# Performance work log

Hardware: AMD Instinct MI355X
Metric: run time of the kernel (lower is better)

The kernel has to match this reference:

```python
import jax, jax.numpy as jnp
import numpy as np

B, C, H, W = 64, 64, 64, 64
KD = 64  # kernel_dim == res == dim (required by the torch reshapes)


def _ln(t, g, b, eps=1e-5):
    mu = jnp.mean(t, axis=-1, keepdims=True)
    var = jnp.var(t, axis=-1, keepdims=True)
    return (t - mu) * jax.lax.rsqrt(var + eps) * g + b


def _cos_map(n, kd):
    i = jnp.arange(n, dtype=jnp.float32)[:, None]
    j = jnp.arange(kd, dtype=jnp.float32)[None, :]
    return jnp.cos(i * j * jnp.pi / n) / kd


def setup_inputs() -> dict:
    key = jax.random.key(0)
    ks = jax.random.split(key, 6)
    s = 0.02
    return {
        "x": jax.random.normal(ks[0], (B, C, H, W), jnp.float32),
        "freq_embed": jax.random.normal(ks[1], (H, W, C), jnp.float32),
        "g_k": jnp.ones((C,), jnp.float32), "b_k": jnp.zeros((C,), jnp.float32),
        "Wk": jax.random.normal(ks[2], (C, KD), jnp.float32) * s, "bk": jnp.zeros((KD,), jnp.float32),
        "g_z": jnp.ones((C,), jnp.float32), "b_z": jnp.zeros((C,), jnp.float32),
        "Wz": jax.random.normal(ks[3], (C, C), jnp.float32) * s, "bz": jnp.zeros((C,), jnp.float32),
        "g_o": jnp.ones((KD,), jnp.float32), "b_o": jnp.zeros((KD,), jnp.float32),
        "Wo": jax.random.normal(ks[4], (KD, C), jnp.float32) * s, "bo": jnp.zeros((C,), jnp.float32),
    }


def reference(x, freq_embed, g_k, b_k, Wk, bk, g_z, b_z, Wz, bz, g_o, b_o, Wo, bo):
    # x: (B,C,H,W) -> (B,H,W,C), matching the torch permute branch
    x = jnp.transpose(x, (0, 2, 3, 1))
    Bc, Hc, Wc, Cc = x.shape
    kd = Wk.shape[1]
    xin = x + freq_embed[None]                    # freq_embed broadcast over batch
    k = _ln(xin, g_k, b_k) @ Wk + bk              # (B,H,W,kd)
    z = _ln(freq_embed, g_z, b_z) @ Wz + bz       # to_k(freq_embed): (H,W,C)
    cosn = _cos_map(Hc, kd)                       # (H,kd)
    cosm = _cos_map(Wc, kd)                       # (W,kd)
    i = jnp.arange(Hc, dtype=jnp.float32)[:, None]
    j = jnp.arange(Wc, dtype=jnp.float32)[None, :]
    decay = (jnp.exp(-(i + j) / max(Hc, Wc)) / kd).astype(x.dtype)  # (H,W)
    wexp = decay[:, :, None] ** z                 # (H,W,C), decay > 0
    # separable forward DCT (two kernel-1 conv1d == two contractions)
    t = jnp.einsum('nh,bhwc->bnwc', cosn, k)
    t = jnp.einsum('mw,bnwc->bnmc', cosm, t)
    t = t * wexp[None]                            # exponential-decay spectral gate
    # separable inverse DCT
    t = jnp.einsum('nh,bnmc->bhmc', cosn, t)
    t = jnp.einsum('mw,bhmc->bhwc', cosm, t)
    out = _ln(t, g_o, b_o) * jax.nn.silu(z)[None]
    out = out @ Wo + bo
    return jnp.transpose(out, (0, 3, 1, 2))       # back to BCHW
```

## Files before the change

### kernel.cpp

```cpp
#include <hip/hip_runtime.h>


typedef __attribute__((ext_vector_type(8))) short short8;
typedef __attribute__((ext_vector_type(4))) float f32x4;
typedef __attribute__((ext_vector_type(4))) unsigned short us4;

__device__ __forceinline__ unsigned short bfhi(float f) {
    return (unsigned short)(__builtin_bit_cast(unsigned int, f) >> 16);
}
__device__ __forceinline__ float hif(float f) {
    return __builtin_bit_cast(float, __builtin_bit_cast(unsigned int, f) & 0xFFFF0000u);
}
__device__ __forceinline__ int swa(int row, int col) {
    return (row << 7) + (((col >> 3) ^ (row & 7)) << 4) + ((col & 7) << 1);
}
__device__ __forceinline__ short8 fragrd(const short* buf, int row, int kc) {
    int a = (row << 7) + ((kc ^ (row & 7)) << 4);
    return *(const short8*)((const char*)buf + a);
}

__device__ __forceinline__ void mm_block(const short* Ah, const short* Al,
                                         const short* Bh, const short* Bl,
                                         int m0, int n0, int l15, int q,
                                         f32x4 (&acc)[2][2]) {
    const f32x4 zero = {0.f, 0.f, 0.f, 0.f};
    acc[0][0] = zero; acc[0][1] = zero; acc[1][0] = zero; acc[1][1] = zero;
    #pragma unroll
    for (int kb = 0; kb < 2; ++kb) {
        int kc = (kb << 2) + q;
        short8 a0h = fragrd(Ah, m0 + l15, kc);
        short8 a0l = fragrd(Al, m0 + l15, kc);
        short8 a1h = fragrd(Ah, m0 + 16 + l15, kc);
        short8 a1l = fragrd(Al, m0 + 16 + l15, kc);
        short8 b0h = fragrd(Bh, n0 + l15, kc);
        short8 b0l = fragrd(Bl, n0 + l15, kc);
        short8 b1h = fragrd(Bh, n0 + 16 + l15, kc);
        short8 b1l = fragrd(Bl, n0 + 16 + l15, kc);
        acc[0][0] = __builtin_amdgcn_mfma_f32_16x16x32_bf16(a0h, b0h, acc[0][0], 0, 0, 0);
        acc[0][0] = __builtin_amdgcn_mfma_f32_16x16x32_bf16(a0h, b0l, acc[0][0], 0, 0, 0);
        acc[0][0] = __builtin_amdgcn_mfma_f32_16x16x32_bf16(a0l, b0h, acc[0][0], 0, 0, 0);
        acc[0][1] = __builtin_amdgcn_mfma_f32_16x16x32_bf16(a0h, b1h, acc[0][1], 0, 0, 0);
        acc[0][1] = __builtin_amdgcn_mfma_f32_16x16x32_bf16(a0h, b1l, acc[0][1], 0, 0, 0);
        acc[0][1] = __builtin_amdgcn_mfma_f32_16x16x32_bf16(a0l, b1h, acc[0][1], 0, 0, 0);
        acc[1][0] = __builtin_amdgcn_mfma_f32_16x16x32_bf16(a1h, b0h, acc[1][0], 0, 0, 0);
        acc[1][0] = __builtin_amdgcn_mfma_f32_16x16x32_bf16(a1h, b0l, acc[1][0], 0, 0, 0);
        acc[1][0] = __builtin_amdgcn_mfma_f32_16x16x32_bf16(a1l, b0h, acc[1][0], 0, 0, 0);
        acc[1][1] = __builtin_amdgcn_mfma_f32_16x16x32_bf16(a1h, b1h, acc[1][1], 0, 0, 0);
        acc[1][1] = __builtin_amdgcn_mfma_f32_16x16x32_bf16(a1h, b1l, acc[1][1], 0, 0, 0);
        acc[1][1] = __builtin_amdgcn_mfma_f32_16x16x32_bf16(a1l, b1h, acc[1][1], 0, 0, 0);
    }
}

__global__ __launch_bounds__(256) void k_pre1(
    const float* __restrict__ g_k, const float* __restrict__ b_k,
    const float* __restrict__ Wk, const float* __restrict__ bk,
    const float* __restrict__ g_z, const float* __restrict__ b_z,
    const float* __restrict__ Wz, const float* __restrict__ bz,
    const float* __restrict__ Wo,
    unsigned short* __restrict__ WkTh, unsigned short* __restrict__ WkTl,
    float* __restrict__ su_k, float* __restrict__ v_k,
    unsigned short* __restrict__ WzTh, unsigned short* __restrict__ WzTl,
    float* __restrict__ su_z, float* __restrict__ v_z,
    unsigned short* __restrict__ WoTh, unsigned short* __restrict__ WoTl,
    unsigned short* __restrict__ cos_hi, unsigned short* __restrict__ cos_lo) {
    int t = threadIdx.x;
    if (blockIdx.x < 16) {
        int n = blockIdx.x * 4 + (t >> 6);
        int c = t & 63;
        float wk = Wk[c * 64 + n];
        float a = g_k[c] * wk;
        WkTh[n * 64 + c] = bfhi(a);
        WkTl[n * 64 + c] = bfhi(a - hif(a));
        float sa = a, sv = b_k[c] * wk;
        #pragma unroll
        for (int off = 32; off > 0; off >>= 1) {
            sa += __shfl_xor(sa, off, 64);
            sv += __shfl_xor(sv, off, 64);
        }
        if (c == 0) { su_k[n] = sa; v_k[n] = sv + bk[n]; }
        float wz = Wz[c * 64 + n];
        float az = g_z[c] * wz;
        WzTh[n * 64 + c] = bfhi(az);
        WzTl[n * 64 + c] = bfhi(az - hif(az));
        float saz = az, svz = b_z[c] * wz;
        #pragma unroll
        for (int off = 32; off > 0; off >>= 1) {
            saz += __shfl_xor(saz, off, 64);
            svz += __shfl_xor(svz, off, 64);
        }
        if (c == 0) { su_z[n] = saz; v_z[n] = svz + bz[n]; }
        float wo = Wo[c * 64 + n];
        WoTh[n * 64 + c] = bfhi(wo);
        WoTl[n * 64 + c] = bfhi(wo - hif(wo));
    } else {
        int idx = (blockIdx.x - 16) * 256 + t;
        int i = idx >> 6, j = idx & 63;
        float ang = (float)(i * j) * 3.14159265358979323846f * (1.0f / 64.0f);
        float v = cosf(ang) * (1.0f / 64.0f);
        cos_hi[idx] = bfhi(v);
        cos_lo[idx] = bfhi(v - hif(v));
    }
}

__global__ __launch_bounds__(256) void k_pre2(
    const float* __restrict__ freq,
    const unsigned short* __restrict__ WzTh_g, const unsigned short* __restrict__ WzTl_g,
    const float* __restrict__ su_z, const float* __restrict__ v_z,
    float* __restrict__ siluzT, float* __restrict__ wexpT,
    float* __restrict__ freqT) {
    __shared__ short Ah[4096], Al[4096], Bh[4096], Bl[4096];
    __shared__ float muS[64], rsS[64];
    __shared__ float tile[64][65];
    int t = threadIdx.x;
    if (blockIdx.x < 64) {
        int h = blockIdx.x;
        #pragma unroll
        for (int p = 0; p < 2; ++p) {
            int e = t + p * 256;
            int row = e >> 3, ch = e & 7;
            int a = (row << 7) + (((ch ^ (row & 7)) << 4));
            *(uint4*)((char*)Bh + a) = *(const uint4*)&WzTh_g[row * 64 + ch * 8];
            *(uint4*)((char*)Bl + a) = *(const uint4*)&WzTl_g[row * 64 + ch * 8];
        }
        int w = t >> 2, c0 = (t & 3) << 4;
        float4 fr[4];
        float s1 = 0.f, s2 = 0.f;
        #pragma unroll
        for (int i = 0; i < 4; ++i) {
            fr[i] = *(const float4*)&freq[(h * 64 + w) * 64 + c0 + 4 * i];
            s1 += fr[i].x + fr[i].y + fr[i].z + fr[i].w;
            s2 += fr[i].x * fr[i].x + fr[i].y * fr[i].y + fr[i].z * fr[i].z + fr[i].w * fr[i].w;
        }
        s1 += __shfl_xor(s1, 1, 64); s1 += __shfl_xor(s1, 2, 64);
        s2 += __shfl_xor(s2, 1, 64); s2 += __shfl_xor(s2, 2, 64);
        float mu = s1 * (1.0f / 64.0f);
        float var = s2 * (1.0f / 64.0f) - mu * mu;
        float rs = rsqrtf(var + 1e-5f);
        if ((t & 3) == 0) { muS[w] = mu; rsS[w] = rs; }
        const float* fp = (const float*)fr;
        #pragma unroll
        for (int i = 0; i < 4; ++i) {
            us4 hv, lv;
            #pragma unroll
            for (int r = 0; r < 4; ++r) {
                float f = fp[i * 4 + r];
                hv[r] = bfhi(f);
                lv[r] = bfhi(f - hif(f));
            }
            int a = swa(w, c0 + 4 * i);
            *(us4*)((char*)Ah + a) = hv;
            *(us4*)((char*)Al + a) = lv;
        }
        __syncthreads();
        int lane = t & 63, wv = t >> 6;
        int q = lane >> 4, l15 = lane & 15;
        int m0 = (wv & 1) << 5, n0 = (wv >> 1) << 5;
        f32x4 acc[2][2];
        mm_block(Ah, Al, Bh, Bl, m0, n0, l15, q, acc);
        #pragma unroll
        for (int u = 0; u < 2; ++u) {
            int c = n0 + (u << 4) + l15;
            float suc = su_z[c], vc = v_z[c];
            #pragma unroll
            for (int ti = 0; ti < 2; ++ti) {
                int wb = m0 + (ti << 4) + (q << 2);
                float4 mu4 = *(const float4*)&muS[wb];
                float4 rs4 = *(const float4*)&rsS[wb];
                float4 sil, wx;
                #pragma unroll
                for (int r = 0; r < 4; ++r) {
                    float z = ((const float*)&rs4)[r] * (acc[ti][u][r] - ((const float*)&mu4)[r] * suc) + vc;
                    float lnd = -(float)(h + wb + r) * 0.015625f - 4.1588830833596718565f;
                    ((float*)&sil)[r] = z / (1.0f + expf(-z));
                    ((float*)&wx)[r] = expf(z * lnd);
                }
                int base = (c * 64 + h) * 64 + wb;
                *(float4*)&siluzT[base] = sil;
                *(float4*)&wexpT[base] = wx;
            }
        }
    } else {
        int h = blockIdx.x - 64;
        int w = t >> 2, c0 = (t & 3) << 4;
        #pragma unroll
        for (int i = 0; i < 4; ++i)
            *(float4*)&tile[w][c0 + 4 * i] = *(const float4*)&freq[(h * 64 + w) * 64 + c0 + 4 * i];
        __syncthreads();
        int w0 = (t & 15) << 2;
        #pragma unroll
        for (int p = 0; p < 4; ++p) {
            int c = (t >> 4) + 16 * p;
            float4 fv = make_float4(tile[w0][c], tile[w0 + 1][c], tile[w0 + 2][c], tile[w0 + 3][c]);
            *(float4*)&freqT[(c * 64 + h) * 64 + w0] = fv;
        }
    }
}

__global__ __launch_bounds__(256, 3) void k_k(
    const float* __restrict__ x, const float* __restrict__ freqT,
    const unsigned short* __restrict__ WkTh_g, const unsigned short* __restrict__ WkTl_g,
    const float* __restrict__ su_k, const float* __restrict__ v_k,
    float* __restrict__ planes) {
    __shared__ short Ah[4096], Al[4096], Bh[4096], Bl[4096];
    __shared__ __align__(16) float red1[16][68], red2[16][68];
    __shared__ float muS[64], rsS[64];
    int b = blockIdx.x >> 6, h = blockIdx.x & 63;
    int t = threadIdx.x;
    #pragma unroll
    for (int p = 0; p < 2; ++p) {
        int e = t + p * 256;
        int row = e >> 3, ch = e & 7;
        int a = (row << 7) + (((ch ^ (row & 7)) << 4));
        *(uint4*)((char*)Bh + a) = *(const uint4*)&WkTh_g[row * 64 + ch * 8];
        *(uint4*)((char*)Bl + a) = *(const uint4*)&WkTl_g[row * 64 + ch * 8];
    }
    int g = t >> 4, w0 = (t & 15) << 2, c0 = g << 2;
    const float* xb = x + (size_t)b * 262144 + h * 64;
    float4 vr[4];
    float4 s1 = {0,0,0,0}, s2 = {0,0,0,0};
    #pragma unroll
    for (int i = 0; i < 4; ++i) {
        int c = c0 + i;
        float4 xv = *(const float4*)&xb[c * 4096 + w0];
        float4 fv = *(const float4*)&freqT[c * 4096 + h * 64 + w0];
        xv.x += fv.x; xv.y += fv.y; xv.z += fv.z; xv.w += fv.w;
        vr[i] = xv;
        s1.x += xv.x; s1.y += xv.y; s1.z += xv.z; s1.w += xv.w;
        s2.x += xv.x * xv.x; s2.y += xv.y * xv.y; s2.z += xv.z * xv.z; s2.w += xv.w * xv.w;
    }
    const float* vp = (const float*)vr;
    #pragma unroll
    for (int j = 0; j < 4; ++j) {
        us4 hv, lv;
        #pragma unroll
        for (int r = 0; r < 4; ++r) {
            float f = vp[r * 4 + j];
            hv[r] = bfhi(f);
            lv[r] = bfhi(f - hif(f));
        }
        int a = swa(w0 + j, c0);
        *(us4*)((char*)Ah + a) = hv;
        *(us4*)((char*)Al + a) = lv;
    }
    *(float4*)&red1[g][w0] = s1;
    *(float4*)&red2[g][w0] = s2;
    __syncthreads();
    if (t < 64) {
        float a1 = 0.f, a2 = 0.f;
        #pragma unroll
        for (int j = 0; j < 16; ++j) { a1 += red1[j][t]; a2 += red2[j][t]; }
        float mu = a1 * (1.0f / 64.0f);
        float var = a2 * (1.0f / 64.0f) - mu * mu;
        muS[t] = mu; rsS[t] = rsqrtf(var + 1e-5f);
    }
    __syncthreads();
    int lane = t & 63, wv = t >> 6;
    int q = lane >> 4, l15 = lane & 15;
    int m0 = (wv & 1) << 5, n0 = (wv >> 1) << 5;
    f32x4 acc[2][2];
    mm_block(Ah, Al, Bh, Bl, m0, n0, l15, q, acc);
    #pragma unroll
    for (int u = 0; u < 2; ++u) {
        int n = n0 + (u << 4) + l15;
        float sun = su_k[n], vn = v_k[n];
        #pragma unroll
        for (int ti = 0; ti < 2; ++ti) {
            int wb = m0 + (ti << 4) + (q << 2);
            float4 mu4 = *(const float4*)&muS[wb];
            float4 rs4 = *(const float4*)&rsS[wb];
            float4 o;
            o.x = rs4.x * (acc[ti][u][0] - mu4.x * sun) + vn;
            o.y = rs4.y * (acc[ti][u][1] - mu4.y * sun) + vn;
            o.z = rs4.z * (acc[ti][u][2] - mu4.z * sun) + vn;
            o.w = rs4.w * (acc[ti][u][3] - mu4.w * sun) + vn;
            *(float4*)&planes[((size_t)(b * 64 + n) * 64 + h) * 64 + wb] = o;
        }
    }
}

__global__ __launch_bounds__(256, 3) void k_spec(
    float* __restrict__ planes,
    const unsigned short* __restrict__ cos_hi, const unsigned short* __restrict__ cos_lo,
    const float* __restrict__ wexpT) {
    __shared__ short Ch[4096], Cl[4096];
    __shared__ short D0h[4096], D0l[4096];
    __shared__ short D1h[4096], D1l[4096];
    int b = blockIdx.x >> 6, c = blockIdx.x & 63;
    float* po = planes + (size_t)(b * 64 + c) * 4096;
    int t = threadIdx.x;
    int lane = t & 63, wv = t >> 6;
    int q = lane >> 4, l15 = lane & 15;
    int m0 = (wv & 1) << 5, n0 = (wv >> 1) << 5;

    {
        int r = t >> 2, cb = (t & 3) << 4;
        #pragma unroll
        for (int p = 0; p < 2; ++p) {
            int chunk = (cb >> 3) + p;
            int a = (r << 7) + (((chunk ^ (r & 7)) << 4));
            *(uint4*)((char*)Ch + a) = *(const uint4*)&cos_hi[r * 64 + cb + p * 8];
            *(uint4*)((char*)Cl + a) = *(const uint4*)&cos_lo[r * 64 + cb + p * 8];
        }
    }
    {
        int w = t & 63, h0 = (t >> 6) << 4;
        float v[16];
        #pragma unroll
        for (int j = 0; j < 16; ++j) v[j] = po[(h0 + j) * 64 + w];
        #pragma unroll
        for (int g = 0; g < 4; ++g) {
            int col = h0 + (g << 2);
            int a = swa(w, col);
            us4 hv, lv;
            #pragma unroll
            for (int r = 0; r < 4; ++r) {
                float f = v[(g << 2) + r];
                hv[r] = bfhi(f);
                lv[r] = bfhi(f - hif(f));
            }
            *(us4*)((char*)D0h + a) = hv;
            *(us4*)((char*)D0l + a) = lv;
        }
    }
    __syncthreads();

    f32x4 acc[2][2];

#define WB_T(Dh, Dl)                                                                \
    {                                                                               \
        _Pragma("unroll")                                                           \
        for (int ti = 0; ti < 2; ++ti)                                              \
            _Pragma("unroll")                                                       \
            for (int u = 0; u < 2; ++u) {                                           \
                int row = n0 + (u << 4) + l15;                                      \
                int col = m0 + (ti << 4) + (q << 2);                                \
                int a = swa(row, col);                                              \
                us4 hv, lv;                                                         \
                _Pragma("unroll")                                                   \
                for (int r = 0; r < 4; ++r) {                                       \
                    float f = acc[ti][u][r];                                        \
                    hv[r] = bfhi(f);                                                \
                    lv[r] = bfhi(f - hif(f));                                       \
                }                                                                   \
                *(us4*)((char*)Dh + a) = hv;                                        \
                *(us4*)((char*)Dl + a) = lv;                                        \
            }                                                                       \
    }

    mm_block(D0h, D0l, Ch, Cl, m0, n0, l15, q, acc);
    WB_T(D1h, D1l)
    __syncthreads();
    mm_block(D1h, D1l, Ch, Cl, m0, n0, l15, q, acc);
    {
        const float* wx = wexpT + (size_t)c * 4096;
        #pragma unroll
        for (int ti = 0; ti < 2; ++ti)
            #pragma unroll
            for (int u = 0; u < 2; ++u)
                #pragma unroll
                for (int r = 0; r < 4; ++r) {
                    int n = m0 + (ti << 4) + (q << 2) + r;
                    int m = n0 + (u << 4) + l15;
                    acc[ti][u][r] *= wx[n * 64 + m];
                }
    }
    WB_T(D0h, D0l)
    __syncthreads();
    mm_block(Ch, Cl, D0h, D0l, m0, n0, l15, q, acc);
    {
        #pragma unroll
        for (int ti = 0; ti < 2; ++ti)
            #pragma unroll
            for (int u = 0; u < 2; ++u)
                #pragma unroll
                for (int r = 0; r < 4; ++r) {
                    int row = m0 + (ti << 4) + (q << 2) + r;
                    int col = n0 + (u << 4) + l15;
                    int a = swa(row, col);
                    float f = acc[ti][u][r];
                    *(unsigned short*)((char*)D1h + a) = bfhi(f);
                    *(unsigned short*)((char*)D1l + a) = bfhi(f - hif(f));
                }
    }
    __syncthreads();
    mm_block(D1h, D1l, Ch, Cl, m0, n0, l15, q, acc);
    {
        #pragma unroll
        for (int ti = 0; ti < 2; ++ti)
            #pragma unroll
            for (int u = 0; u < 2; ++u)
                #pragma unroll
                for (int r = 0; r < 4; ++r) {
                    int h = m0 + (ti << 4) + (q << 2) + r;
                    int w = n0 + (u << 4) + l15;
                    po[h * 64 + w] = acc[ti][u][r];
                }
    }
#undef WB_T
}

__global__ __launch_bounds__(256, 3) void k_out(
    const float* __restrict__ planes, const float* __restrict__ siluzT,
    const float* __restrict__ g_o, const float* __restrict__ b_o,
    const unsigned short* __restrict__ WoTh_g, const unsigned short* __restrict__ WoTl_g,
    const float* __restrict__ bo, float* __restrict__ out) {
    __shared__ short Ah[4096], Al[4096], Bh[4096], Bl[4096];
    __shared__ __align__(16) float red1[16][68], red2[16][68];
    __shared__ float muS[64], rsS[64];
    int b = blockIdx.x >> 6, h = blockIdx.x & 63;
    int t = threadIdx.x;
    #pragma unroll
    for (int p = 0; p < 2; ++p) {
        int e = t + p * 256;
        int row = e >> 3, ch = e & 7;
        int a = (row << 7) + (((ch ^ (row & 7)) << 4));
        *(uint4*)((char*)Bh + a) = *(const uint4*)&WoTh_g[row * 64 + ch * 8];
        *(uint4*)((char*)Bl + a) = *(const uint4*)&WoTl_g[row * 64 + ch * 8];
    }
    int g = t >> 4, w0 = (t & 15) << 2, c0 = g << 2;
    const float* pb = planes + (size_t)b * 262144 + h * 64;
    float4 vr[4], szr[4];
    float4 s1 = {0,0,0,0}, s2 = {0,0,0,0};
    #pragma unroll
    for (int i = 0; i < 4; ++i) {
        int c = c0 + i;
        float4 tv = *(const float4*)&pb[c * 4096 + w0];
        szr[i] = *(const float4*)&siluzT[c * 4096 + h * 64 + w0];
        vr[i] = tv;
        s1.x += tv.x; s1.y += tv.y; s1.z += tv.z; s1.w += tv.w;
        s2.x += tv.x * tv.x; s2.y += tv.y * tv.y; s2.z += tv.z * tv.z; s2.w += tv.w * tv.w;
    }
    *(float4*)&red1[g][w0] = s1;
    *(float4*)&red2[g][w0] = s2;
    __syncthreads();
    if (t < 64) {
        float a1 = 0.f, a2 = 0.f;
        #pragma unroll
        for (int j = 0; j < 16; ++j) { a1 += red1[j][t]; a2 += red2[j][t]; }
        float mu = a1 * (1.0f / 64.0f);
        float var = a2 * (1.0f / 64.0f) - mu * mu;
        muS[t] = mu; rsS[t] = rsqrtf(var + 1e-5f);
    }
    __syncthreads();
    {
        float4 mu4 = *(const float4*)&muS[w0];
        float4 rs4 = *(const float4*)&rsS[w0];
        #pragma unroll
        for (int i = 0; i < 4; ++i) {
            int c = c0 + i;
            float go = g_o[c], boc = b_o[c];
            vr[i].x = ((vr[i].x - mu4.x) * rs4.x * go + boc) * szr[i].x;
            vr[i].y = ((vr[i].y - mu4.y) * rs4.y * go + boc) * szr[i].y;
            vr[i].z = ((vr[i].z - mu4.z) * rs4.z * go + boc) * szr[i].z;
            vr[i].w = ((vr[i].w - mu4.w) * rs4.w * go + boc) * szr[i].w;
        }
        const float* vp = (const float*)vr;
        #pragma unroll
        for (int j = 0; j < 4; ++j) {
            us4 hv, lv;
            #pragma unroll
            for (int r = 0; r < 4; ++r) {
                float f = vp[r * 4 + j];
                hv[r] = bfhi(f);
                lv[r] = bfhi(f - hif(f));
            }
            int a = swa(w0 + j, c0);
            *(us4*)((char*)Ah + a) = hv;
            *(us4*)((char*)Al + a) = lv;
        }
    }
    __syncthreads();
    int lane = t & 63, wv = t >> 6;
    int q = lane >> 4, l15 = lane & 15;
    int m0 = (wv & 1) << 5, n0 = (wv >> 1) << 5;
    f32x4 acc[2][2];
    mm_block(Ah, Al, Bh, Bl, m0, n0, l15, q, acc);
    #pragma unroll
    for (int u = 0; u < 2; ++u) {
        int o_ = n0 + (u << 4) + l15;
        float bov = bo[o_];
        #pragma unroll
        for (int ti = 0; ti < 2; ++ti) {
            int wb = m0 + (ti << 4) + (q << 2);
            float4 o;
            o.x = acc[ti][u][0] + bov;
            o.y = acc[ti][u][1] + bov;
            o.z = acc[ti][u][2] + bov;
            o.w = acc[ti][u][3] + bov;
            *(float4*)&out[((size_t)(b * 64 + o_) * 64 + h) * 64 + wb] = o;
        }
    }
}

extern "C" void kernel_launch(void* const* d_in, const int* in_sizes, int n_in,
                              void* d_out, int out_size, void* d_ws, size_t ws_size,
                              hipStream_t stream) {
    const float* x    = (const float*)d_in[0];
    const float* freq = (const float*)d_in[1];
    const float* g_k  = (const float*)d_in[2];
    const float* b_k  = (const float*)d_in[3];
    const float* Wk   = (const float*)d_in[4];
    const float* bk   = (const float*)d_in[5];
    const float* g_z  = (const float*)d_in[6];
    const float* b_z  = (const float*)d_in[7];
    const float* Wz   = (const float*)d_in[8];
    const float* bz   = (const float*)d_in[9];
    const float* g_o  = (const float*)d_in[10];
    const float* b_o  = (const float*)d_in[11];
    const float* Wo   = (const float*)d_in[12];
    const float* bo   = (const float*)d_in[13];
    float* out = (float*)d_out;

    float* ws = (float*)d_ws;
    float* planes = ws;
    float* siluzT = planes + 16777216;
    float* wexpT  = siluzT + 262144;
    float* freqT  = wexpT + 262144;
    float* su_k   = freqT + 262144;
    float* v_k    = su_k + 64;
    float* su_z   = v_k + 64;
    float* v_z    = su_z + 64;
    unsigned short* cos_hi = (unsigned short*)(v_z + 64);
    unsigned short* cos_lo = cos_hi + 4096;
    unsigned short* WkTh = cos_lo + 4096;
    unsigned short* WkTl = WkTh + 4096;
    unsigned short* WzTh = WkTl + 4096;
    unsigned short* WzTl = WzTh + 4096;
    unsigned short* WoTh = WzTl + 4096;
    unsigned short* WoTl = WoTh + 4096;

    k_pre1<<<32, 256, 0, stream>>>(g_k, b_k, Wk, bk, g_z, b_z, Wz, bz, Wo,
                                   WkTh, WkTl, su_k, v_k, WzTh, WzTl, su_z, v_z,
                                   WoTh, WoTl, cos_hi, cos_lo);
    k_pre2<<<128, 256, 0, stream>>>(freq, WzTh, WzTl, su_z, v_z, siluzT, wexpT, freqT);
    k_k<<<4096, 256, 0, stream>>>(x, freqT, WkTh, WkTl, su_k, v_k, planes);
    k_spec<<<4096, 256, 0, stream>>>(planes, cos_hi, cos_lo, wexpT);
    k_out<<<4096, 256, 0, stream>>>(planes, siluzT, g_o, b_o, WoTh, WoTl, bo, out);
}
```

Before: 210.7 us.

## Move bf16 hi/lo split into k_k epilogue and shuffle-reduce LN stats in double

k_k now stores the k planes as packed bf16 hi/lo pairs, so k_spec only unpacks bits when loading instead of recomputing the split. The LayerNorm statistics in k_pre2, k_k and k_out are accumulated in double. In k_k and k_out a wavefront shuffle reduction feeds a small shared array, which removes one __syncthreads and the serial 64-thread reduction step. Occupancy hints for k_k and k_out are raised from 3 to 4. Double-precision arithmetic and shuffles add FP64 ALU cost, and the packed planes hold only the bf16 hi+lo precision.

```diff
diff --git a/kernel.cpp b/kernel.cpp
--- a/kernel.cpp
+++ b/kernel.cpp
@@ -10,6 +10,11 @@
 }
 __device__ __forceinline__ float hif(float f) {
     return __builtin_bit_cast(float, __builtin_bit_cast(unsigned int, f) & 0xFFFF0000u);
+}
+__device__ __forceinline__ unsigned int packsplit(float f) {
+    unsigned int h = (unsigned int)bfhi(f);
+    unsigned int l = (unsigned int)bfhi(f - hif(f));
+    return (h << 16) | l;
 }
 __device__ __forceinline__ int swa(int row, int col) {
     return (row << 7) + (((col >> 3) ^ (row & 7)) << 4) + ((col & 7) << 1);
@@ -124,19 +129,23 @@
         }
         int w = t >> 2, c0 = (t & 3) << 4;
         float4 fr[4];
-        float s1 = 0.f, s2 = 0.f;
+        double s1 = 0.0, s2 = 0.0;
         #pragma unroll
         for (int i = 0; i < 4; ++i) {
             fr[i] = *(const float4*)&freq[(h * 64 + w) * 64 + c0 + 4 * i];
-            s1 += fr[i].x + fr[i].y + fr[i].z + fr[i].w;
-            s2 += fr[i].x * fr[i].x + fr[i].y * fr[i].y + fr[i].z * fr[i].z + fr[i].w * fr[i].w;
+            const float* fp = (const float*)&fr[i];
+            #pragma unroll
+            for (int r = 0; r < 4; ++r) {
+                double d = (double)fp[r];
+                s1 += d; s2 += d * d;
+            }
         }
         s1 += __shfl_xor(s1, 1, 64); s1 += __shfl_xor(s1, 2, 64);
         s2 += __shfl_xor(s2, 1, 64); s2 += __shfl_xor(s2, 2, 64);
-        float mu = s1 * (1.0f / 64.0f);
-        float var = s2 * (1.0f / 64.0f) - mu * mu;
-        float rs = rsqrtf(var + 1e-5f);
-        if ((t & 3) == 0) { muS[w] = mu; rsS[w] = rs; }
+        double mu = s1 * (1.0 / 64.0);
+        double var = s2 * (1.0 / 64.0) - mu * mu;
+        float rs = rsqrtf((float)(var + 1e-5));
+        if ((t & 3) == 0) { muS[w] = (float)mu; rsS[w] = rs; }
         const float* fp = (const float*)fr;
         #pragma unroll
         for (int i = 0; i < 4; ++i) {
@@ -196,16 +205,17 @@
     }
 }
 
-__global__ __launch_bounds__(256, 3) void k_k(
+__global__ __launch_bounds__(256, 4) void k_k(
     const float* __restrict__ x, const float* __restrict__ freqT,
     const unsigned short* __restrict__ WkTh_g, const unsigned short* __restrict__ WkTl_g,
     const float* __restrict__ su_k, const float* __restrict__ v_k,
-    float* __restrict__ planes) {
+    unsigned int* __restrict__ planes) {
     __shared__ short Ah[4096], Al[4096], Bh[4096], Bl[4096];
-    __shared__ __align__(16) float red1[16][68], red2[16][68];
-    __shared__ float muS[64], rsS[64];
+    __shared__ double red1[4][64], red2[4][64];
     int b = blockIdx.x >> 6, h = blockIdx.x & 63;
     int t = threadIdx.x;
+    int lane = t & 63, wv = t >> 6;
+    int q = lane >> 4, l15 = lane & 15;
     #pragma unroll
     for (int p = 0; p < 2; ++p) {
         int e = t + p * 256;
@@ -217,7 +227,7 @@
     int g = t >> 4, w0 = (t & 15) << 2, c0 = g << 2;
     const float* xb = x + (size_t)b * 262144 + h * 64;
     float4 vr[4];
-    float4 s1 = {0,0,0,0}, s2 = {0,0,0,0};
+    double s1[4] = {0,0,0,0}, s2[4] = {0,0,0,0};
     #pragma unroll
     for (int i = 0; i < 4; ++i) {
         int c = c0 + i;
@@ -225,8 +235,27 @@
         float4 fv = *(const float4*)&freqT[c * 4096 + h * 64 + w0];
         xv.x += fv.x; xv.y += fv.y; xv.z += fv.z; xv.w += fv.w;
         vr[i] = xv;
-        s1.x += xv.x; s1.y += xv.y; s1.z += xv.z; s1.w += xv.w;
-        s2.x += xv.x * xv.x; s2.y += xv.y * xv.y; s2.z += xv.z * xv.z; s2.w += xv.w * xv.w;
+        const float* xp = (const float*)&xv;
+        #pragma unroll
+        for (int r = 0; r < 4; ++r) {
+            double d = (double)xp[r];
+            s1[r] += d; s2[r] += d * d;
+        }
+    }
+    #pragma unroll
+    for (int off = 16; off <= 32; off <<= 1) {
+        #pragma unroll
+        for (int r = 0; r < 4; ++r) {
+            s1[r] += __shfl_xor(s1[r], off, 64);
+            s2[r] += __shfl_xor(s2[r], off, 64);
+        }
+    }
+    if (q == 0) {
+        #pragma unroll
+        for (int r = 0; r < 4; ++r) {
+            red1[wv][(l15 << 2) + r] = s1[r];
+            red2[wv][(l15 << 2) + r] = s2[r];
+        }
     }
     const float* vp = (const float*)vr;
     #pragma unroll
@@ -242,51 +271,47 @@
         *(us4*)((char*)Ah + a) = hv;
         *(us4*)((char*)Al + a) = lv;
     }
-    *(float4*)&red1[g][w0] = s1;
-    *(float4*)&red2[g][w0] = s2;
-    __syncthreads();
-    if (t < 64) {
-        float a1 = 0.f, a2 = 0.f;
-        #pragma unroll
-        for (int j = 0; j < 16; ++j) { a1 += red1[j][t]; a2 += red2[j][t]; }
-        float mu = a1 * (1.0f / 64.0f);
-        float var = a2 * (1.0f / 64.0f) - mu * mu;
-        muS[t] = mu; rsS[t] = rsqrtf(var + 1e-5f);
-    }
-    __syncthreads();
-    int lane = t & 63, wv = t >> 6;
-    int q = lane >> 4, l15 = lane & 15;
+    __syncthreads();
     int m0 = (wv & 1) << 5, n0 = (wv >> 1) << 5;
     f32x4 acc[2][2];
     mm_block(Ah, Al, Bh, Bl, m0, n0, l15, q, acc);
     #pragma unroll
-    for (int u = 0; u < 2; ++u) {
-        int n = n0 + (u << 4) + l15;
-        float sun = su_k[n], vn = v_k[n];
-        #pragma unroll
-        for (int ti = 0; ti < 2; ++ti) {
-            int wb = m0 + (ti << 4) + (q << 2);
-            float4 mu4 = *(const float4*)&muS[wb];
-            float4 rs4 = *(const float4*)&rsS[wb];
-            float4 o;
-            o.x = rs4.x * (acc[ti][u][0] - mu4.x * sun) + vn;
-            o.y = rs4.y * (acc[ti][u][1] - mu4.y * sun) + vn;
-            o.z = rs4.z * (acc[ti][u][2] - mu4.z * sun) + vn;
-            o.w = rs4.w * (acc[ti][u][3] - mu4.w * sun) + vn;
-            *(float4*)&planes[((size_t)(b * 64 + n) * 64 + h) * 64 + wb] = o;
+    for (int ti = 0; ti < 2; ++ti) {
+        int wb = m0 + (ti << 4) + (q << 2);
+        float4 mu4, rs4;
+        #pragma unroll
+        for (int r = 0; r < 4; ++r) {
+            double a1 = red1[0][wb + r] + red1[1][wb + r] + red1[2][wb + r] + red1[3][wb + r];
+            double a2 = red2[0][wb + r] + red2[1][wb + r] + red2[2][wb + r] + red2[3][wb + r];
+            double mu = a1 * (1.0 / 64.0);
+            double var = a2 * (1.0 / 64.0) - mu * mu;
+            ((float*)&mu4)[r] = (float)mu;
+            ((float*)&rs4)[r] = rsqrtf((float)(var + 1e-5));
+        }
+        #pragma unroll
+        for (int u = 0; u < 2; ++u) {
+            int n = n0 + (u << 4) + l15;
+            float sun = su_k[n], vn = v_k[n];
+            uint4 o;
+            o.x = packsplit(rs4.x * (acc[ti][u][0] - mu4.x * sun) + vn);
+            o.y = packsplit(rs4.y * (acc[ti][u][1] - mu4.y * sun) + vn);
+            o.z = packsplit(rs4.z * (acc[ti][u][2] - mu4.z * sun) + vn);
+            o.w = packsplit(rs4.w * (acc[ti][u][3] - mu4.w * sun) + vn);
+            *(uint4*)&planes[((size_t)(b * 64 + n) * 64 + h) * 64 + wb] = o;
         }
     }
 }
 
 __global__ __launch_bounds__(256, 3) void k_spec(
-    float* __restrict__ planes,
+    unsigned int* __restrict__ planes,
     const unsigned short* __restrict__ cos_hi, const unsigned short* __restrict__ cos_lo,
     const float* __restrict__ wexpT) {
     __shared__ short Ch[4096], Cl[4096];
     __shared__ short D0h[4096], D0l[4096];
     __shared__ short D1h[4096], D1l[4096];
     int b = blockIdx.x >> 6, c = blockIdx.x & 63;
-    float* po = planes + (size_t)(b * 64 + c) * 4096;
+    unsigned int* pu = planes + (size_t)(b * 64 + c) * 4096;
+    float* po = (float*)pu;
     int t = threadIdx.x;
     int lane = t & 63, wv = t >> 6;
     int q = lane >> 4, l15 = lane & 15;
@@ -304,9 +329,9 @@
     }
     {
         int w = t & 63, h0 = (t >> 6) << 4;
-        float v[16];
-        #pragma unroll
-        for (int j = 0; j < 16; ++j) v[j] = po[(h0 + j) * 64 + w];
+        unsigned int v[16];
+        #pragma unroll
+        for (int j = 0; j < 16; ++j) v[j] = pu[(h0 + j) * 64 + w];
         #pragma unroll
         for (int g = 0; g < 4; ++g) {
             int col = h0 + (g << 2);
@@ -314,9 +339,9 @@
             us4 hv, lv;
             #pragma unroll
             for (int r = 0; r < 4; ++r) {
-                float f = v[(g << 2) + r];
-                hv[r] = bfhi(f);
-                lv[r] = bfhi(f - hif(f));
+                unsigned int pv = v[(g << 2) + r];
+                hv[r] = (unsigned short)(pv >> 16);
+                lv[r] = (unsigned short)(pv & 0xFFFFu);
             }
             *(us4*)((char*)D0h + a) = hv;
             *(us4*)((char*)D0l + a) = lv;
@@ -399,16 +424,17 @@
 #undef WB_T
 }
 
-__global__ __launch_bounds__(256, 3) void k_out(
+__global__ __launch_bounds__(256, 4) void k_out(
     const float* __restrict__ planes, const float* __restrict__ siluzT,
     const float* __restrict__ g_o, const float* __restrict__ b_o,
     const unsigned short* __restrict__ WoTh_g, const unsigned short* __restrict__ WoTl_g,
     const float* __restrict__ bo, float* __restrict__ out) {
     __shared__ short Ah[4096], Al[4096], Bh[4096], Bl[4096];
-    __shared__ __align__(16) float red1[16][68], red2[16][68];
-    __shared__ float muS[64], rsS[64];
+    __shared__ double red1[4][64], red2[4][64];
     int b = blockIdx.x >> 6, h = blockIdx.x & 63;
     int t = threadIdx.x;
+    int lane = t & 63, wv = t >> 6;
+    int q = lane >> 4, l15 = lane & 15;
     #pragma unroll
     for (int p = 0; p < 2; ++p) {
         int e = t + p * 256;
@@ -420,31 +446,47 @@
     int g = t >> 4, w0 = (t & 15) << 2, c0 = g << 2;
     const float* pb = planes + (size_t)b * 262144 + h * 64;
     float4 vr[4], szr[4];
-    float4 s1 = {0,0,0,0}, s2 = {0,0,0,0};
+    double s1[4] = {0,0,0,0}, s2[4] = {0,0,0,0};
     #pragma unroll
     for (int i = 0; i < 4; ++i) {
         int c = c0 + i;
         float4 tv = *(const float4*)&pb[c * 4096 + w0];
         szr[i] = *(const float4*)&siluzT[c * 4096 + h * 64 + w0];
         vr[i] = tv;
-        s1.x += tv.x; s1.y += tv.y; s1.z += tv.z; s1.w += tv.w;
-        s2.x += tv.x * tv.x; s2.y += tv.y * tv.y; s2.z += tv.z * tv.z; s2.w += tv.w * tv.w;
-    }
-    *(float4*)&red1[g][w0] = s1;
-    *(float4*)&red2[g][w0] = s2;
-    __syncthreads();
-    if (t < 64) {
-        float a1 = 0.f, a2 = 0.f;
-        #pragma unroll
-        for (int j = 0; j < 16; ++j) { a1 += red1[j][t]; a2 += red2[j][t]; }
-        float mu = a1 * (1.0f / 64.0f);
-        float var = a2 * (1.0f / 64.0f) - mu * mu;
-        muS[t] = mu; rsS[t] = rsqrtf(var + 1e-5f);
+        const float* xp = (const float*)&tv;
+        #pragma unroll
+        for (int r = 0; r < 4; ++r) {
+            double d = (double)xp[r];
+            s1[r] += d; s2[r] += d * d;
+        }
+    }
+    #pragma unroll
+    for (int off = 16; off <= 32; off <<= 1) {
+        #pragma unroll
+        for (int r = 0; r < 4; ++r) {
+            s1[r] += __shfl_xor(s1[r], off, 64);
+            s2[r] += __shfl_xor(s2[r], off, 64);
+        }
+    }
+    if (q == 0) {
+        #pragma unroll
+        for (int r = 0; r < 4; ++r) {
+            red1[wv][(l15 << 2) + r] = s1[r];
+            red2[wv][(l15 << 2) + r] = s2[r];
+        }
     }
     __syncthreads();
     {
-        float4 mu4 = *(const float4*)&muS[w0];
-        float4 rs4 = *(const float4*)&rsS[w0];
+        float4 mu4, rs4;
+        #pragma unroll
+        for (int r = 0; r < 4; ++r) {
+            double a1 = red1[0][w0 + r] + red1[1][w0 + r] + red1[2][w0 + r] + red1[3][w0 + r];
+            double a2 = red2[0][w0 + r] + red2[1][w0 + r] + red2[2][w0 + r] + red2[3][w0 + r];
+            double mu = a1 * (1.0 / 64.0);
+            double var = a2 * (1.0 / 64.0) - mu * mu;
+            ((float*)&mu4)[r] = (float)mu;
+            ((float*)&rs4)[r] = rsqrtf((float)(var + 1e-5));
+        }
         #pragma unroll
         for (int i = 0; i < 4; ++i) {
             int c = c0 + i;
@@ -470,8 +512,6 @@
         }
     }
     __syncthreads();
-    int lane = t & 63, wv = t >> 6;
-    int q = lane >> 4, l15 = lane & 15;
     int m0 = (wv & 1) << 5, n0 = (wv >> 1) << 5;
     f32x4 acc[2][2];
     mm_block(Ah, Al, Bh, Bl, m0, n0, l15, q, acc);
@@ -533,7 +573,7 @@
                                    WkTh, WkTl, su_k, v_k, WzTh, WzTl, su_z, v_z,
                                    WoTh, WoTl, cos_hi, cos_lo);
     k_pre2<<<128, 256, 0, stream>>>(freq, WzTh, WzTl, su_z, v_z, siluzT, wexpT, freqT);
-    k_k<<<4096, 256, 0, stream>>>(x, freqT, WkTh, WkTl, su_k, v_k, planes);
-    k_spec<<<4096, 256, 0, stream>>>(planes, cos_hi, cos_lo, wexpT);
+    k_k<<<4096, 256, 0, stream>>>(x, freqT, WkTh, WkTl, su_k, v_k, (unsigned int*)planes);
+    k_spec<<<4096, 256, 0, stream>>>((unsigned int*)planes, cos_hi, cos_lo, wexpT);
     k_out<<<4096, 256, 0, stream>>>(planes, siluzT, g_o, b_o, WoTh, WoTl, bo, out);
 }
```

Measured after the change: 218.6 us. 3.8% more time.
